# Kernel tuning notes

Hardware: AMD Instinct MI355X
Metric: run time of the kernel (lower is better)

Reference implementation:

```python
import jax, jax.numpy as jnp
import numpy as np

FEAT_DIM = 2048
HIDDEN = 1024
ATTN_DIM = 512
BATCH = 128
NPOS = 196


def setup_inputs() -> dict:
    key = jax.random.key(0)
    ks = jax.random.split(key, 8)
    # Linear layers use kaiming-uniform-ish init; plain scaled normal is fine for a numeric baseline.
    def lin(k, fan_in, fan_out):
        k1, k2 = jax.random.split(k)
        bound = 1.0 / np.sqrt(fan_in)
        W = jax.random.uniform(k1, (fan_out, fan_in), jnp.float32, -bound, bound)
        b = jax.random.uniform(k2, (fan_out,), jnp.float32, -bound, bound)
        return W, b
    We, be = lin(ks[0], FEAT_DIM, ATTN_DIM)
    Wd, bd = lin(ks[1], HIDDEN, ATTN_DIM)
    Wf, bf = lin(ks[2], ATTN_DIM, 1)
    encoder_out = jax.random.normal(ks[3], (BATCH, NPOS, FEAT_DIM), jnp.float32)
    hidden = jax.random.normal(ks[4], (BATCH, HIDDEN), jnp.float32)
    return {
        "encoder_out": encoder_out,
        "hidden": hidden,
        "We": We, "be": be,
        "Wd": Wd, "bd": bd,
        "Wf": Wf, "bf": bf,
    }


def reference(encoder_out, hidden, We, be, Wd, bd, Wf, bf):
    # enc: [B, P, A]; dec: [B, 1, A]
    enc = jnp.einsum('bpf,af->bpa', encoder_out, We) + be
    dec = (jnp.einsum('bh,ah->ba', hidden, Wd) + bd)[:, None, :]
    scores = jnp.tanh(enc + dec)
    # full_attn: [A] -> scalar per position; Wf has shape [1, A]
    scores = jnp.einsum('bpa,a->bp', scores, Wf[0]) + bf[0]
    alpha = jax.nn.softmax(scores, axis=1)  # [B, P]
    context = jnp.einsum('bpf,bp->bf', encoder_out, alpha)  # [B, F]
    return context, alpha
```

## Files before the change

### kernel.cpp

```cpp
#include <hip/hip_runtime.h>
#include <hip/hip_bf16.h>

typedef __bf16 bf16x8 __attribute__((ext_vector_type(8)));
typedef __bf16 bf16x4 __attribute__((ext_vector_type(4)));
typedef float f32x4 __attribute__((ext_vector_type(4)));

#define FEAT 2048
#define HID  1024
#define AD   512
#define NB   128
#define NP   196
#define MROWS (NB * NP)
#define BM 128
#define BN 128
#define BK 64
#define NSTEP (FEAT / BK)
#define NBLK (MROWS / BM * 4)

__global__ __launch_bounds__(256) void pack_we_k(const float* __restrict__ We,
                                                 __bf16* __restrict__ Bp) {
    int t = blockIdx.x * 256 + threadIdx.x;
    int a  = t >> 8;
    int f0 = (t & 255) << 3;
    const float4* src = reinterpret_cast<const float4*>(We + ((size_t)a << 11) + f0);
    float4 x0 = src[0], x1 = src[1];
    int nt = a >> 4, r = a & 15;
    int kt = f0 >> 5, g = (f0 >> 3) & 3;
    size_t off = (((size_t)(kt * 32 + nt) * 64) + (r + (g << 4))) << 3;
    union { __bf16 h[8]; bf16x8 v; } u;
    u.h[0] = (__bf16)x0.x; u.h[1] = (__bf16)x0.y; u.h[2] = (__bf16)x0.z; u.h[3] = (__bf16)x0.w;
    u.h[4] = (__bf16)x1.x; u.h[5] = (__bf16)x1.y; u.h[6] = (__bf16)x1.z; u.h[7] = (__bf16)x1.w;
    *reinterpret_cast<bf16x8*>(Bp + off) = u.v;
}

__global__ __launch_bounds__(256) void dec_k(const float* __restrict__ hidden,
                                             const float* __restrict__ Wd,
                                             const float* __restrict__ bd,
                                             const float* __restrict__ be,
                                             float* __restrict__ decb) {
    __shared__ float w[8][1028];
    const int tid = threadIdx.x;
    const int n0 = blockIdx.x << 3;
    const float4* wsrc = reinterpret_cast<const float4*>(Wd + ((size_t)n0 << 10));
    #pragma unroll
    for (int i = 0; i < 8; ++i)
        *reinterpret_cast<float4*>(&w[i][tid << 2]) = wsrc[(i << 8) + tid];
    __syncthreads();
    const int nl = tid & 7, b0 = tid >> 3;
    float acc[4] = {0.f, 0.f, 0.f, 0.f};
    const float4* wp = reinterpret_cast<const float4*>(&w[nl][0]);
    #pragma unroll 2
    for (int k4 = 0; k4 < 256; ++k4) {
        float4 wv = wp[k4];
        #pragma unroll
        for (int i = 0; i < 4; ++i) {
            const float4 h = reinterpret_cast<const float4*>(
                hidden + ((size_t)(b0 + (i << 5)) << 10))[k4];
            acc[i] = fmaf(wv.x, h.x, acc[i]);
            acc[i] = fmaf(wv.y, h.y, acc[i]);
            acc[i] = fmaf(wv.z, h.z, acc[i]);
            acc[i] = fmaf(wv.w, h.w, acc[i]);
        }
    }
    const float bias = bd[n0 + nl] + be[n0 + nl];
    #pragma unroll
    for (int i = 0; i < 4; ++i)
        decb[(size_t)(b0 + (i << 5)) * AD + n0 + nl] = acc[i] + bias;
}

__global__ __launch_bounds__(256, 3) void enc_score_k(
        const float* __restrict__ X, const __bf16* __restrict__ Bp,
        const float* __restrict__ decb, const float* __restrict__ Wf,
        float* __restrict__ spart) {
    __shared__ char Asm[2][BM * BK * 2];
    __shared__ float swave[2][BM];
    const int tid  = threadIdx.x;
    const int wave = tid >> 6, lane = tid & 63;
    const int lr = lane & 15, lg = lane >> 4;
    const int wm = wave >> 1, wn = wave & 1;
    const int vbid = (blockIdx.x & 7) * 98 + (blockIdx.x >> 3);
    const int rt = vbid >> 2, nq = vbid & 3;
    const int row0 = rt * BM;
    const int ncol0 = nq * BN + wn * 64;

    f32x4 acc[4][4];
    #pragma unroll
    for (int mt = 0; mt < 4; ++mt) {
        #pragma unroll
        for (int j = 0; j < 4; ++j) {
            const int row = wm * 64 + mt * 16 + lg * 4 + j;
            const int b = (unsigned)(row0 + row) / 196u;
            const float* dp = decb + (size_t)b * AD + ncol0 + lr;
            #pragma unroll
            for (int nt = 0; nt < 4; ++nt) acc[mt][nt][j] = dp[nt * 16];
        }
    }

    const int srow = tid >> 4;
    const int schk = tid & 15;
    const float* gA = X + (size_t)(row0 + srow) * FEAT + schk * 4;
    const int rswz = (lr & 7) << 4;
    const __bf16* Bq = Bp + ((size_t)(nq * 8 + wn * 4) << 9) + (lane << 3);

    float4 rA[8];
    #pragma unroll
    for (int i = 0; i < 8; ++i)
        rA[i] = *reinterpret_cast<const float4*>(gA + (size_t)(i * 16) * FEAT);
    #pragma unroll
    for (int i = 0; i < 8; ++i) {
        const int r = srow + 16 * i;
        union { __bf16 h[4]; bf16x4 v; } p;
        p.h[0] = (__bf16)rA[i].x; p.h[1] = (__bf16)rA[i].y;
        p.h[2] = (__bf16)rA[i].z; p.h[3] = (__bf16)rA[i].w;
        *reinterpret_cast<bf16x4*>(Asm[0] + r * 128 + ((schk * 8) ^ ((r & 7) << 4))) = p.v;
    }
    __syncthreads();

    int cur = 0;
    for (int t = 0; t < NSTEP; ++t) {
        if (t + 1 < NSTEP) {
            const float* g = gA + (size_t)(t + 1) * BK;
            #pragma unroll
            for (int i = 0; i < 8; ++i)
                rA[i] = *reinterpret_cast<const float4*>(g + (size_t)(i * 16) * FEAT);
        }
        #pragma unroll
        for (int kt2 = 0; kt2 < 2; ++kt2) {
            const size_t kt = 2 * t + kt2;
            bf16x8 bfr[4];
            #pragma unroll
            for (int j = 0; j < 4; ++j)
                bfr[j] = *reinterpret_cast<const bf16x8*>(Bq + kt * 16384 + j * 512);
            #pragma unroll
            for (int mt = 0; mt < 4; ++mt) {
                const int R = wm * 64 + mt * 16 + lr;
                bf16x8 a = *reinterpret_cast<const bf16x8*>(
                    Asm[cur] + R * 128 + ((kt2 * 64 + lg * 16) ^ rswz));
                acc[mt][0] = __builtin_amdgcn_mfma_f32_16x16x32_bf16(a, bfr[0], acc[mt][0], 0, 0, 0);
                acc[mt][1] = __builtin_amdgcn_mfma_f32_16x16x32_bf16(a, bfr[1], acc[mt][1], 0, 0, 0);
                acc[mt][2] = __builtin_amdgcn_mfma_f32_16x16x32_bf16(a, bfr[2], acc[mt][2], 0, 0, 0);
                acc[mt][3] = __builtin_amdgcn_mfma_f32_16x16x32_bf16(a, bfr[3], acc[mt][3], 0, 0, 0);
            }
        }
        if (t + 1 < NSTEP) {
            #pragma unroll
            for (int i = 0; i < 8; ++i) {
                const int r = srow + 16 * i;
                union { __bf16 h[4]; bf16x4 v; } p;
                p.h[0] = (__bf16)rA[i].x; p.h[1] = (__bf16)rA[i].y;
                p.h[2] = (__bf16)rA[i].z; p.h[3] = (__bf16)rA[i].w;
                *reinterpret_cast<bf16x4*>(
                    Asm[cur ^ 1] + r * 128 + ((schk * 8) ^ ((r & 7) << 4))) = p.v;
            }
        }
        __syncthreads();
        cur ^= 1;
    }

    float wf[4];
    #pragma unroll
    for (int nt = 0; nt < 4; ++nt) wf[nt] = Wf[ncol0 + nt * 16 + lr];
    #pragma unroll
    for (int mt = 0; mt < 4; ++mt) {
        #pragma unroll
        for (int j = 0; j < 4; ++j) {
            float s = 0.f;
            #pragma unroll
            for (int nt = 0; nt < 4; ++nt) {
                float x = acc[mt][nt][j];
                float e = __expf(2.0f * x);
                float t = 1.0f - 2.0f / (e + 1.0f);
                s = fmaf(t, wf[nt], s);
            }
            s += __shfl_xor(s, 1); s += __shfl_xor(s, 2);
            s += __shfl_xor(s, 4); s += __shfl_xor(s, 8);
            if (lr == 0) swave[wn][wm * 64 + mt * 16 + lg * 4 + j] = s;
        }
    }
    __syncthreads();
    if (tid < BM)
        spart[(size_t)nq * MROWS + row0 + tid] = swave[0][tid] + swave[1][tid];
}

__global__ __launch_bounds__(64) void softmax_k(const float* __restrict__ spart,
                                                float* __restrict__ alpha) {
    const int b = blockIdx.x, lane = threadIdx.x;
    float v[4], e[4];
    float m = -3.0e38f;
    #pragma unroll
    for (int i = 0; i < 4; ++i) {
        int p = i * 64 + lane;
        if (p < NP) {
            int idx = b * NP + p;
            v[i] = spart[idx] + spart[MROWS + idx] + spart[2 * MROWS + idx]
                 + spart[3 * MROWS + idx];
        } else v[i] = -3.0e38f;
        m = fmaxf(m, v[i]);
    }
    #pragma unroll
    for (int o = 1; o < 64; o <<= 1) m = fmaxf(m, __shfl_xor(m, o));
    float s = 0.f;
    #pragma unroll
    for (int i = 0; i < 4; ++i) {
        int p = i * 64 + lane;
        e[i] = (p < NP) ? __expf(v[i] - m) : 0.f;
        s += e[i];
    }
    #pragma unroll
    for (int o = 1; o < 64; o <<= 1) s += __shfl_xor(s, o);
    const float inv = 1.0f / s;
    #pragma unroll
    for (int i = 0; i < 4; ++i) {
        int p = i * 64 + lane;
        if (p < NP) alpha[b * NP + p] = e[i] * inv;
    }
}

__global__ __launch_bounds__(128) void context_k(const float* __restrict__ X,
                                                 const float* __restrict__ alpha,
                                                 float* __restrict__ ctx) {
    __shared__ float al[NP];
    const int bid = blockIdx.x;
    const int b = 127 - (bid >> 2);
    const int chunk = bid & 3;
    const int tid = threadIdx.x;
    for (int i = tid; i < NP; i += 128) al[i] = alpha[b * NP + i];
    __syncthreads();
    const float4* Xp = reinterpret_cast<const float4*>(X + (size_t)b * NP * FEAT)
                       + chunk * 128 + tid;
    float4 a0 = {0,0,0,0}, a1 = {0,0,0,0};
    #pragma unroll 4
    for (int p = 0; p < NP; p += 2) {
        const float w0 = al[p], w1 = al[p + 1];
        const float4 x0 = Xp[(size_t)p * 512];
        const float4 x1 = Xp[(size_t)(p + 1) * 512];
        a0.x = fmaf(w0, x0.x, a0.x); a0.y = fmaf(w0, x0.y, a0.y);
        a0.z = fmaf(w0, x0.z, a0.z); a0.w = fmaf(w0, x0.w, a0.w);
        a1.x = fmaf(w1, x1.x, a1.x); a1.y = fmaf(w1, x1.y, a1.y);
        a1.z = fmaf(w1, x1.z, a1.z); a1.w = fmaf(w1, x1.w, a1.w);
    }
    float4 rr; rr.x = a0.x + a1.x; rr.y = a0.y + a1.y; rr.z = a0.z + a1.z; rr.w = a0.w + a1.w;
    *reinterpret_cast<float4*>(ctx + (size_t)b * FEAT + chunk * 512 + tid * 4) = rr;
}

extern "C" void kernel_launch(void* const* d_in, const int* in_sizes, int n_in,
                              void* d_out, int out_size, void* d_ws, size_t ws_size,
                              hipStream_t stream) {
    const float* enc    = (const float*)d_in[0];
    const float* hidden = (const float*)d_in[1];
    const float* We     = (const float*)d_in[2];
    const float* be     = (const float*)d_in[3];
    const float* Wd     = (const float*)d_in[4];
    const float* bd     = (const float*)d_in[5];
    const float* Wf     = (const float*)d_in[6];

    float* out   = (float*)d_out;
    float* ctx   = out;
    float* alpha = out + NB * FEAT;

    char* ws = (char*)d_ws;
    __bf16* Bp    = (__bf16*)ws;
    float*  decb  = (float*)(ws + (2u << 20));
    float*  spart = (float*)(ws + (2u << 20) + (256u << 10));

    pack_we_k  <<<dim3(512), dim3(256), 0, stream>>>(We, Bp);
    dec_k      <<<dim3(64),  dim3(256), 0, stream>>>(hidden, Wd, bd, be, decb);
    enc_score_k<<<dim3(NBLK), dim3(256), 0, stream>>>(enc, Bp, decb, Wf, spart);
    softmax_k  <<<dim3(NB),  dim3(64),  0, stream>>>(spart, alpha);
    context_k  <<<dim3(512), dim3(128), 0, stream>>>(enc, alpha, ctx);
}
```

Before: 192.2 us.

## Stream fp32 A tiles into LDS via global_load_lds and convert at fragment read

Replaces the register-staged, bf16-converting double-buffered A load with direct global-to-LDS 16-byte loads (global_load_lds) into a single fp32 LDS tile using an XOR swizzle. The fp32-to-bf16 conversion moves to the LDS fragment read inside the MFMA loop, and B fragments are now register double-buffered one step ahead. This removes VGPR staging and LDS write instructions, at the cost of a single LDS buffer that serialises global loads with compute, twice the LDS footprint and more LDS read traffic per MFMA.

```diff
diff --git a/kernel.cpp b/kernel.cpp
--- a/kernel.cpp
+++ b/kernel.cpp
@@ -2,7 +2,6 @@
 #include <hip/hip_bf16.h>
 
 typedef __bf16 bf16x8 __attribute__((ext_vector_type(8)));
-typedef __bf16 bf16x4 __attribute__((ext_vector_type(4)));
 typedef float f32x4 __attribute__((ext_vector_type(4)));
 
 #define FEAT 2048
@@ -16,6 +15,12 @@
 #define BK 64
 #define NSTEP (FEAT / BK)
 #define NBLK (MROWS / BM * 4)
+
+__device__ __forceinline__ void gload16(const void* g, void* l) {
+    __builtin_amdgcn_global_load_lds(
+        (const __attribute__((address_space(1))) void*)(g),
+        (__attribute__((address_space(3))) void*)(l), 16, 0, 0);
+}
 
 __global__ __launch_bounds__(256) void pack_we_k(const float* __restrict__ We,
                                                  __bf16* __restrict__ Bp) {
@@ -68,11 +73,41 @@
         decb[(size_t)(b0 + (i << 5)) * AD + n0 + nl] = acc[i] + bias;
 }
 
+__device__ __forceinline__ void load_b(const __bf16* bs, bf16x8 f[8]) {
+    #pragma unroll
+    for (int kt2 = 0; kt2 < 2; ++kt2)
+        #pragma unroll
+        for (int j = 0; j < 4; ++j)
+            f[kt2 * 4 + j] = *reinterpret_cast<const bf16x8*>(bs + kt2 * 16384 + j * 512);
+}
+
+__device__ __forceinline__ void compute_step(const char* As, const bf16x8 f[8],
+                                             int wm, int lr, int lg, f32x4 acc[4][4]) {
+    #pragma unroll
+    for (int kt2 = 0; kt2 < 2; ++kt2) {
+        #pragma unroll
+        for (int mt = 0; mt < 4; ++mt) {
+            const int R = wm * 64 + mt * 16 + lr;
+            const int key = (R & 15) << 4;
+            const int x0 = (kt2 * 128 + lg * 32) ^ key;
+            const float4 a0 = *reinterpret_cast<const float4*>(As + R * 256 + x0);
+            const float4 a1 = *reinterpret_cast<const float4*>(As + R * 256 + (x0 ^ 16));
+            union { __bf16 h[8]; bf16x8 v; } pa;
+            pa.h[0]=(__bf16)a0.x; pa.h[1]=(__bf16)a0.y; pa.h[2]=(__bf16)a0.z; pa.h[3]=(__bf16)a0.w;
+            pa.h[4]=(__bf16)a1.x; pa.h[5]=(__bf16)a1.y; pa.h[6]=(__bf16)a1.z; pa.h[7]=(__bf16)a1.w;
+            acc[mt][0] = __builtin_amdgcn_mfma_f32_16x16x32_bf16(pa.v, f[kt2*4+0], acc[mt][0], 0, 0, 0);
+            acc[mt][1] = __builtin_amdgcn_mfma_f32_16x16x32_bf16(pa.v, f[kt2*4+1], acc[mt][1], 0, 0, 0);
+            acc[mt][2] = __builtin_amdgcn_mfma_f32_16x16x32_bf16(pa.v, f[kt2*4+2], acc[mt][2], 0, 0, 0);
+            acc[mt][3] = __builtin_amdgcn_mfma_f32_16x16x32_bf16(pa.v, f[kt2*4+3], acc[mt][3], 0, 0, 0);
+        }
+    }
+}
+
 __global__ __launch_bounds__(256, 3) void enc_score_k(
         const float* __restrict__ X, const __bf16* __restrict__ Bp,
         const float* __restrict__ decb, const float* __restrict__ Wf,
         float* __restrict__ spart) {
-    __shared__ char Asm[2][BM * BK * 2];
+    __shared__ __align__(16) char As[BM * BK * 4];
     __shared__ float swave[2][BM];
     const int tid  = threadIdx.x;
     const int wave = tid >> 6, lane = tid & 63;
@@ -96,65 +131,37 @@
         }
     }
 
-    const int srow = tid >> 4;
-    const int schk = tid & 15;
-    const float* gA = X + (size_t)(row0 + srow) * FEAT + schk * 4;
-    const int rswz = (lr & 7) << 4;
+    const char* Xb = (const char*)X;
+    unsigned aoff[8];
+    char* aldsp[8];
+    #pragma unroll
+    for (int i = 0; i < 8; ++i) {
+        const int row = wave * 32 + i * 4 + (lane >> 4);
+        aoff[i] = (unsigned)(row0 + row) * (FEAT * 4)
+                + (((lane & 15) * 16) ^ ((row & 15) << 4));
+        aldsp[i] = As + wave * 8192 + i * 1024;
+    }
     const __bf16* Bq = Bp + ((size_t)(nq * 8 + wn * 4) << 9) + (lane << 3);
 
-    float4 rA[8];
-    #pragma unroll
-    for (int i = 0; i < 8; ++i)
-        rA[i] = *reinterpret_cast<const float4*>(gA + (size_t)(i * 16) * FEAT);
-    #pragma unroll
-    for (int i = 0; i < 8; ++i) {
-        const int r = srow + 16 * i;
-        union { __bf16 h[4]; bf16x4 v; } p;
-        p.h[0] = (__bf16)rA[i].x; p.h[1] = (__bf16)rA[i].y;
-        p.h[2] = (__bf16)rA[i].z; p.h[3] = (__bf16)rA[i].w;
-        *reinterpret_cast<bf16x4*>(Asm[0] + r * 128 + ((schk * 8) ^ ((r & 7) << 4))) = p.v;
-    }
-    __syncthreads();
-
-    int cur = 0;
-    for (int t = 0; t < NSTEP; ++t) {
-        if (t + 1 < NSTEP) {
-            const float* g = gA + (size_t)(t + 1) * BK;
-            #pragma unroll
-            for (int i = 0; i < 8; ++i)
-                rA[i] = *reinterpret_cast<const float4*>(g + (size_t)(i * 16) * FEAT);
-        }
-        #pragma unroll
-        for (int kt2 = 0; kt2 < 2; ++kt2) {
-            const size_t kt = 2 * t + kt2;
-            bf16x8 bfr[4];
-            #pragma unroll
-            for (int j = 0; j < 4; ++j)
-                bfr[j] = *reinterpret_cast<const bf16x8*>(Bq + kt * 16384 + j * 512);
-            #pragma unroll
-            for (int mt = 0; mt < 4; ++mt) {
-                const int R = wm * 64 + mt * 16 + lr;
-                bf16x8 a = *reinterpret_cast<const bf16x8*>(
-                    Asm[cur] + R * 128 + ((kt2 * 64 + lg * 16) ^ rswz));
-                acc[mt][0] = __builtin_amdgcn_mfma_f32_16x16x32_bf16(a, bfr[0], acc[mt][0], 0, 0, 0);
-                acc[mt][1] = __builtin_amdgcn_mfma_f32_16x16x32_bf16(a, bfr[1], acc[mt][1], 0, 0, 0);
-                acc[mt][2] = __builtin_amdgcn_mfma_f32_16x16x32_bf16(a, bfr[2], acc[mt][2], 0, 0, 0);
-                acc[mt][3] = __builtin_amdgcn_mfma_f32_16x16x32_bf16(a, bfr[3], acc[mt][3], 0, 0, 0);
-            }
-        }
-        if (t + 1 < NSTEP) {
-            #pragma unroll
-            for (int i = 0; i < 8; ++i) {
-                const int r = srow + 16 * i;
-                union { __bf16 h[4]; bf16x4 v; } p;
-                p.h[0] = (__bf16)rA[i].x; p.h[1] = (__bf16)rA[i].y;
-                p.h[2] = (__bf16)rA[i].z; p.h[3] = (__bf16)rA[i].w;
-                *reinterpret_cast<bf16x4*>(
-                    Asm[cur ^ 1] + r * 128 + ((schk * 8) ^ ((r & 7) << 4))) = p.v;
-            }
-        }
+    bf16x8 bfrA[8], bfrB[8];
+    load_b(Bq, bfrA);
+
+    #pragma unroll 1
+    for (int t2 = 0; t2 < NSTEP; t2 += 2) {
+        __builtin_amdgcn_s_barrier();
+        #pragma unroll
+        for (int i = 0; i < 8; ++i)
+            gload16(Xb + (size_t)aoff[i] + (size_t)t2 * 256, aldsp[i]);
         __syncthreads();
-        cur ^= 1;
+        load_b(Bq + (size_t)(t2 + 1) * 32768, bfrB);
+        compute_step(As, bfrA, wm, lr, lg, acc);
+        __builtin_amdgcn_s_barrier();
+        #pragma unroll
+        for (int i = 0; i < 8; ++i)
+            gload16(Xb + (size_t)aoff[i] + (size_t)(t2 + 1) * 256, aldsp[i]);
+        __syncthreads();
+        if (t2 + 2 < NSTEP) load_b(Bq + (size_t)(t2 + 2) * 32768, bfrA);
+        compute_step(As, bfrB, wm, lr, lg, acc);
     }
 
     float wf[4];
```

Result: slower. 271.6 us (+41.4%).
